# Kernel tuning notes

Measured on AMD Instinct MI355X. Metric: run time of the kernel, lower is better.

The kernel has to match this reference:

```python
import jax, jax.numpy as jnp
import numpy as np

MAX_ARMY_SEND = 64


def setup_inputs() -> dict:
    key = jax.random.key(0)
    ks = jax.random.split(key, 12)
    N, D, E = 100000, 128, 1000000
    H = 128            # hidden_dim (== embed_dim)
    AH = 128           # army_scorer hidden width (hardcoded 128 in the module)
    node_embeddings = jax.random.normal(ks[0], (N, D), dtype=jnp.float32)
    action_edges = jax.random.randint(ks[1], (E, 2), 0, N, dtype=jnp.int32)
    army_counts = jax.random.randint(ks[2], (N,), 0, 50, dtype=jnp.int32)
    s = lambda fan_in: 1.0 / np.sqrt(fan_in)
    # edge_scorer: Linear(2H -> H), ReLU, Linear(H -> 1)
    W1 = jax.random.uniform(ks[3], (2 * H, H), jnp.float32, -s(2 * H), s(2 * H))
    b1 = jnp.zeros((H,), jnp.float32)
    W2 = jax.random.uniform(ks[4], (H, 1), jnp.float32, -s(H), s(H))
    b2 = jnp.zeros((1,), jnp.float32)
    # army_scorer: Linear(2D -> 128), ReLU, Linear(128 -> max_army_send)
    A1 = jax.random.uniform(ks[5], (2 * D, AH), jnp.float32, -s(2 * D), s(2 * D))
    ab1 = jnp.zeros((AH,), jnp.float32)
    A2 = jax.random.uniform(ks[6], (AH, MAX_ARMY_SEND), jnp.float32, -s(AH), s(AH))
    ab2 = jnp.zeros((MAX_ARMY_SEND,), jnp.float32)
    return {
        "node_embeddings": node_embeddings,
        "action_edges": action_edges,
        "army_counts": army_counts,
        "W1": W1, "b1": b1, "W2": W2, "b2": b2,
        "A1": A1, "ab1": ab1, "A2": A2, "ab2": ab2,
    }


def reference(node_embeddings, action_edges, army_counts,
              W1, b1, W2, b2, A1, ab1, A2, ab2):
    src = action_edges[:, 0]
    tgt = action_edges[:, 1]
    # irregular gather: [E, 2D]
    edge_embed = jnp.concatenate([node_embeddings[src], node_embeddings[tgt]], axis=-1)
    # edge scorer MLP -> [E]
    h = jax.nn.relu(edge_embed @ W1 + b1)
    edge_logits = (h @ W2 + b2)[:, 0]
    # army scorer MLP -> [E, max_army_send]
    ha = jax.nn.relu(edge_embed @ A1 + ab1)
    army_logits = ha @ A2 + ab2
    # masking
    src_armies = army_counts[src]
    tgt_armies = army_counts[tgt]
    bad_edges = (src_armies <= 2) | (tgt_armies >= 3 * src_armies)
    edge_logits = edge_logits - bad_edges.astype(jnp.float32) * 1.0
    edge_logits = edge_logits - (src == tgt).astype(jnp.float32) * 100.0
    max_sendable = src_armies - 1                     # [E]
    army_range = jnp.arange(MAX_ARMY_SEND)[None, :]   # [1, K]
    valid_mask = army_range <= max_sendable[:, None]  # [E, K]
    army_logits = jnp.where(valid_mask, army_logits, jnp.float32(-1000000000.0))
    return edge_logits, army_logits
```

## Files before the change

kernel.cpp:

```cpp
#include <hip/hip_runtime.h>
#include <stdint.h>

typedef __bf16 bf16x8 __attribute__((ext_vector_type(8)));
typedef float floatx4 __attribute__((ext_vector_type(4)));
typedef float floatx2 __attribute__((ext_vector_type(2)));

#define LDP 136
#define LDP8 136

__device__ __forceinline__ float bf2f(unsigned short u) {
  return __uint_as_float(((unsigned)u) << 16);
}
__device__ __forceinline__ unsigned short f2bf(float f) {
  unsigned x = __float_as_uint(f);
  unsigned r = (x + 0x7fffu + ((x >> 16) & 1u)) >> 16;
  return (unsigned short)r;
}
__device__ __forceinline__ unsigned char f2fp8(float x) {
  int p = __builtin_amdgcn_cvt_pk_fp8_f32(x, 0.f, 0, false);
  return (unsigned char)(p & 0xff);
}

union LLU { uint2 u2; long long ll; };

__global__ __launch_bounds__(256) void k_convert_emb(
    const float* __restrict__ src, unsigned short* __restrict__ dst, int n4) {
  int i = blockIdx.x * 256 + threadIdx.x;
  if (i >= n4) return;
  float4 v = ((const float4*)src)[i];
  ushort4 o;
  o.x = f2bf(v.x); o.y = f2bf(v.y); o.z = f2bf(v.z); o.w = f2bf(v.w);
  ((ushort4*)dst)[i] = o;
}

__global__ __launch_bounds__(256) void k_prep_weights(
    const float* __restrict__ W1, const float* __restrict__ A1,
    const float* __restrict__ A2,
    unsigned short* __restrict__ WcatT, unsigned char* __restrict__ A2T8) {
  int idx = blockIdx.x * 256 + threadIdx.x;
  if (idx < 512 * 128) {
    int j = idx >> 7, k = idx & 127;
    float v;
    if (j < 128)      v = W1[k * 128 + j];
    else if (j < 256) v = A1[k * 128 + (j - 128)];
    else if (j < 384) v = W1[(128 + k) * 128 + (j - 256)];
    else              v = A1[(128 + k) * 128 + (j - 384)];
    WcatT[idx] = f2bf(v);
  } else if (idx < 512 * 128 + 64 * 128) {
    int i = idx - 512 * 128;
    int n = i >> 7, k = i & 127;
    A2T8[i] = f2fp8(A2[k * 64 + n]);
  }
}

__global__ __launch_bounds__(256, 3) void k_precompute(
    const unsigned short* __restrict__ emb,
    const unsigned short* __restrict__ WcatT,
    unsigned char* __restrict__ P8,
    int N) {
  __shared__ __align__(16) unsigned short a_lds[64 * LDP];
  __shared__ __align__(16) unsigned short b_lds[128 * LDP];
  const int t = threadIdx.x;
  const int m0 = (blockIdx.x >> 2) * 64;
  const int j0 = (blockIdx.x & 3) * 128;

  for (int it = 0; it < 4; ++it) {
    int i = it * 256 + t;
    int row = i >> 4, c8 = (i & 15) * 8;
    uint4 v = make_uint4(0u, 0u, 0u, 0u);
    if (m0 + row < N) v = *(const uint4*)(emb + (size_t)(m0 + row) * 128 + c8);
    *(uint4*)&a_lds[row * LDP + c8] = v;
  }
  for (int it = 0; it < 8; ++it) {
    int i = it * 256 + t;
    int jr = i >> 4, c8 = (i & 15) * 8;
    uint4 v = *(const uint4*)(WcatT + (size_t)(j0 + jr) * 128 + c8);
    *(uint4*)&b_lds[jr * LDP + c8] = v;
  }
  __syncthreads();

  const int w = t >> 6, l = t & 63;
  const int lr = l & 15, quad = l >> 4;
  floatx4 acc[8];
  for (int nt = 0; nt < 8; ++nt) acc[nt] = (floatx4){0.f, 0.f, 0.f, 0.f};
  for (int ks = 0; ks < 4; ++ks) {
    bf16x8 af = *(const bf16x8*)&a_lds[(w * 16 + lr) * LDP + ks * 32 + quad * 8];
    for (int nt = 0; nt < 8; ++nt) {
      bf16x8 bfv = *(const bf16x8*)&b_lds[(nt * 16 + lr) * LDP + ks * 32 + quad * 8];
      acc[nt] = __builtin_amdgcn_mfma_f32_16x16x32_bf16(af, bfv, acc[nt], 0, 0, 0);
    }
  }
  for (int nt = 0; nt < 8; ++nt) {
    int col = j0 + nt * 16 + lr;
    for (int r = 0; r < 4; ++r) {
      int n = m0 + w * 16 + quad * 4 + r;
      if (n < N) P8[(size_t)n * 512 + col] = f2fp8(acc[nt][r]);
    }
  }
}

__global__ __launch_bounds__(256, 6) void k_edges(
    const unsigned char* __restrict__ P8,
    const unsigned char* __restrict__ A2T8g,
    const int* __restrict__ edges,
    const int* __restrict__ army,
    const float* __restrict__ b1, const float* __restrict__ ab1,
    const float* __restrict__ W2, const float* __restrict__ b2,
    const float* __restrict__ ab2,
    float* __restrict__ out_edge,
    float* __restrict__ out_army,
    int E) {
  __shared__ __align__(16) unsigned char ha8[64 * LDP8];
  __shared__ __align__(16) unsigned char a2t8[64 * LDP8];
  __shared__ float s_b1cat[256];
  __shared__ float s_w2[128];
  __shared__ float s_ab2[64];
  __shared__ int s_army[64];
  __shared__ int s_edges[128];

  const int t = threadIdx.x;
  const int e0 = blockIdx.x * 64;

  for (int it = 0; it < 2; ++it) {
    int i = it * 256 + t;
    int n = i >> 3, c = (i & 7) * 16;
    *(uint4*)&a2t8[n * LDP8 + c] = *(const uint4*)(A2T8g + n * 128 + c);
  }
  s_b1cat[t] = (t < 128) ? b1[t] : ab1[t - 128];
  if (t < 128) {
    s_w2[t] = W2[t];
    int ei = e0 * 2 + t;
    s_edges[t] = (ei < E * 2) ? edges[ei] : 0;
  }
  if (t < 64) s_ab2[t] = ab2[t];
  __syncthreads();

  const float b2v = b2[0];
  const int lp = t & 31;
  const int eh = t >> 5;
  const int j0 = lp * 8;
  float rb[8], rw[8];
#pragma unroll
  for (int i = 0; i < 8; ++i) rb[i] = s_b1cat[j0 + i];
  if (lp < 16) {
#pragma unroll
    for (int i = 0; i < 8; ++i) rw[i] = s_w2[j0 + i];
  }
  for (int it = 0; it < 8; ++it) {
    int el = it * 8 + eh;
    if (e0 + el >= E) continue;
    int src = s_edges[el * 2];
    int tgt = s_edges[el * 2 + 1];
    uint2 us = *(const uint2*)(P8 + (size_t)src * 512 + j0);
    uint2 ut = *(const uint2*)(P8 + (size_t)tgt * 512 + 256 + j0);
    floatx2 s01 = __builtin_amdgcn_cvt_pk_f32_fp8(us.x, false);
    floatx2 s23 = __builtin_amdgcn_cvt_pk_f32_fp8(us.x, true);
    floatx2 s45 = __builtin_amdgcn_cvt_pk_f32_fp8(us.y, false);
    floatx2 s67 = __builtin_amdgcn_cvt_pk_f32_fp8(us.y, true);
    floatx2 t01 = __builtin_amdgcn_cvt_pk_f32_fp8(ut.x, false);
    floatx2 t23 = __builtin_amdgcn_cvt_pk_f32_fp8(ut.x, true);
    floatx2 t45 = __builtin_amdgcn_cvt_pk_f32_fp8(ut.y, false);
    floatx2 t67 = __builtin_amdgcn_cvt_pk_f32_fp8(ut.y, true);
    float h[8];
    h[0] = s01.x + t01.x + rb[0]; h[1] = s01.y + t01.y + rb[1];
    h[2] = s23.x + t23.x + rb[2]; h[3] = s23.y + t23.y + rb[3];
    h[4] = s45.x + t45.x + rb[4]; h[5] = s45.y + t45.y + rb[5];
    h[6] = s67.x + t67.x + rb[6]; h[7] = s67.y + t67.y + rb[7];
#pragma unroll
    for (int i = 0; i < 8; ++i) h[i] = h[i] > 0.f ? h[i] : 0.f;
    if (lp < 16) {
      float part = 0.f;
#pragma unroll
      for (int i = 0; i < 8; ++i) part += h[i] * rw[i];
      part += __shfl_down(part, 8, 16);
      part += __shfl_down(part, 4, 16);
      part += __shfl_down(part, 2, 16);
      part += __shfl_down(part, 1, 16);
      if (lp == 0) {
        int sa = army[src], ta = army[tgt];
        float logit = part + b2v;
        if (sa <= 2 || ta >= 3 * sa) logit -= 1.f;
        if (src == tgt) logit -= 100.f;
        out_edge[e0 + el] = logit;
        s_army[el] = sa;
      }
    } else {
      unsigned o0 = (unsigned)__builtin_amdgcn_cvt_pk_fp8_f32(h[0], h[1], 0, false);
      o0 = (unsigned)__builtin_amdgcn_cvt_pk_fp8_f32(h[2], h[3], (int)o0, true);
      unsigned o1 = (unsigned)__builtin_amdgcn_cvt_pk_fp8_f32(h[4], h[5], 0, false);
      o1 = (unsigned)__builtin_amdgcn_cvt_pk_fp8_f32(h[6], h[7], (int)o1, true);
      *(uint2*)&ha8[el * LDP8 + (j0 - 128)] = make_uint2(o0, o1);
    }
  }
  __syncthreads();

  const int w = t >> 6, l = t & 63;
  const int lr = l & 15, quad = l >> 4;
  floatx4 acc[4];
  for (int nt = 0; nt < 4; ++nt) acc[nt] = (floatx4){0.f, 0.f, 0.f, 0.f};
  for (int ks = 0; ks < 4; ++ks) {
    LLU av;
    av.u2 = *(const uint2*)&ha8[(w * 16 + lr) * LDP8 + ks * 32 + quad * 8];
#pragma unroll
    for (int nt = 0; nt < 4; ++nt) {
      LLU bv;
      bv.u2 = *(const uint2*)&a2t8[(nt * 16 + lr) * LDP8 + ks * 32 + quad * 8];
      acc[nt] = __builtin_amdgcn_mfma_f32_16x16x32_fp8_fp8(av.ll, bv.ll, acc[nt], 0, 0, 0);
    }
  }
#pragma unroll
  for (int nt = 0; nt < 4; ++nt) {
    int col = nt * 16 + lr;
    float bias = s_ab2[col];
#pragma unroll
    for (int r = 0; r < 4; ++r) {
      int el = w * 16 + quad * 4 + r;
      if (e0 + el >= E) continue;
      int sa = s_army[el];
      float v = acc[nt][r] + bias;
      v = (col < sa) ? v : -1e9f;
      out_army[(size_t)(e0 + el) * 64 + col] = v;
    }
  }
}

extern "C" void kernel_launch(void* const* d_in, const int* in_sizes, int n_in,
                              void* d_out, int out_size, void* d_ws, size_t ws_size,
                              hipStream_t stream) {
  const float* emb_f = (const float*)d_in[0];
  const int* edges   = (const int*)d_in[1];
  const int* army    = (const int*)d_in[2];
  const float* W1    = (const float*)d_in[3];
  const float* b1    = (const float*)d_in[4];
  const float* W2    = (const float*)d_in[5];
  const float* b2    = (const float*)d_in[6];
  const float* A1    = (const float*)d_in[7];
  const float* ab1   = (const float*)d_in[8];
  const float* A2    = (const float*)d_in[9];
  const float* ab2   = (const float*)d_in[10];

  const int N = in_sizes[0] / 128;
  const int E = in_sizes[1] / 2;

  char* ws = (char*)d_ws;
  unsigned short* emb_bf = (unsigned short*)ws;
  unsigned short* WcatT  = (unsigned short*)(ws + (size_t)N * 256);
  unsigned char*  A2T8   = (unsigned char*)(WcatT + 512 * 128);
  unsigned char*  P8     = A2T8 + 64 * 128;

  float* out_edge = (float*)d_out;
  float* out_army = out_edge + E;

  int n4 = (N * 128) / 4;
  hipLaunchKernelGGL(k_convert_emb, dim3((n4 + 255) / 256), dim3(256), 0, stream,
                     emb_f, emb_bf, n4);
  hipLaunchKernelGGL(k_prep_weights, dim3((512 * 128 + 64 * 128 + 255) / 256), dim3(256),
                     0, stream, W1, A1, A2, WcatT, A2T8);
  hipLaunchKernelGGL(k_precompute, dim3(((N + 63) / 64) * 4), dim3(256), 0, stream,
                     emb_bf, WcatT, P8, N);
  hipLaunchKernelGGL(k_edges, dim3((E + 63) / 64), dim3(256), 0, stream,
                     P8, A2T8, edges, army, b1, ab1, W2, b2, ab2,
                     out_edge, out_army, E);
}
```

Measured before the change: 459.6 us.

## Fuse embedding bf16 conversion into precompute and stage fp8 output through LDS

Removes the separate fp32-to-bf16 embedding conversion kernel and converts on load inside the precompute GEMM, saving a full write and re-read of the bf16 embedding buffer plus a launch. The fp8 results are staged in shared memory and written out as coalesced 16-byte rows instead of scattered single-byte stores. It also raises the edge kernel's occupancy hint from 6 to 8 blocks. In exchange, each of the four column blocks per row tile now re-reads and re-converts fp32 embeddings, doubling load bytes into precompute, and the higher occupancy hint may cause register spills in the edge kernel.

```diff
diff --git a/kernel.cpp b/kernel.cpp
--- a/kernel.cpp
+++ b/kernel.cpp
@@ -7,10 +7,8 @@
 
 #define LDP 136
 #define LDP8 136
-
-__device__ __forceinline__ float bf2f(unsigned short u) {
-  return __uint_as_float(((unsigned)u) << 16);
-}
+#define CST 144
+
 __device__ __forceinline__ unsigned short f2bf(float f) {
   unsigned x = __float_as_uint(f);
   unsigned r = (x + 0x7fffu + ((x >> 16) & 1u)) >> 16;
@@ -22,16 +20,6 @@
 }
 
 union LLU { uint2 u2; long long ll; };
-
-__global__ __launch_bounds__(256) void k_convert_emb(
-    const float* __restrict__ src, unsigned short* __restrict__ dst, int n4) {
-  int i = blockIdx.x * 256 + threadIdx.x;
-  if (i >= n4) return;
-  float4 v = ((const float4*)src)[i];
-  ushort4 o;
-  o.x = f2bf(v.x); o.y = f2bf(v.y); o.z = f2bf(v.z); o.w = f2bf(v.w);
-  ((ushort4*)dst)[i] = o;
-}
 
 __global__ __launch_bounds__(256) void k_prep_weights(
     const float* __restrict__ W1, const float* __restrict__ A1,
@@ -54,22 +42,27 @@
 }
 
 __global__ __launch_bounds__(256, 3) void k_precompute(
-    const unsigned short* __restrict__ emb,
+    const float* __restrict__ emb_f,
     const unsigned short* __restrict__ WcatT,
     unsigned char* __restrict__ P8,
     int N) {
-  __shared__ __align__(16) unsigned short a_lds[64 * LDP];
-  __shared__ __align__(16) unsigned short b_lds[128 * LDP];
+  __shared__ __align__(16) unsigned char smem[64 * LDP * 2 + 128 * LDP * 2];
+  unsigned short* a_lds = (unsigned short*)smem;
+  unsigned short* b_lds = (unsigned short*)(smem + 64 * LDP * 2);
+  unsigned char*  c_lds = smem;
+
   const int t = threadIdx.x;
   const int m0 = (blockIdx.x >> 2) * 64;
   const int j0 = (blockIdx.x & 3) * 128;
 
-  for (int it = 0; it < 4; ++it) {
-    int i = it * 256 + t;
-    int row = i >> 4, c8 = (i & 15) * 8;
-    uint4 v = make_uint4(0u, 0u, 0u, 0u);
-    if (m0 + row < N) v = *(const uint4*)(emb + (size_t)(m0 + row) * 128 + c8);
-    *(uint4*)&a_lds[row * LDP + c8] = v;
+  for (int it = 0; it < 8; ++it) {
+    int i = it * 256 + t;
+    int row = i >> 5, c4 = (i & 31) * 4;
+    float4 v = make_float4(0.f, 0.f, 0.f, 0.f);
+    if (m0 + row < N) v = *(const float4*)(emb_f + (size_t)(m0 + row) * 128 + c4);
+    ushort4 o;
+    o.x = f2bf(v.x); o.y = f2bf(v.y); o.z = f2bf(v.z); o.w = f2bf(v.w);
+    *(ushort4*)&a_lds[row * LDP + c4] = o;
   }
   for (int it = 0; it < 8; ++it) {
     int i = it * 256 + t;
@@ -85,21 +78,36 @@
   for (int nt = 0; nt < 8; ++nt) acc[nt] = (floatx4){0.f, 0.f, 0.f, 0.f};
   for (int ks = 0; ks < 4; ++ks) {
     bf16x8 af = *(const bf16x8*)&a_lds[(w * 16 + lr) * LDP + ks * 32 + quad * 8];
+#pragma unroll
     for (int nt = 0; nt < 8; ++nt) {
       bf16x8 bfv = *(const bf16x8*)&b_lds[(nt * 16 + lr) * LDP + ks * 32 + quad * 8];
       acc[nt] = __builtin_amdgcn_mfma_f32_16x16x32_bf16(af, bfv, acc[nt], 0, 0, 0);
     }
   }
+  __syncthreads();
+
+#pragma unroll
   for (int nt = 0; nt < 8; ++nt) {
-    int col = j0 + nt * 16 + lr;
+    int col = nt * 16 + lr;
+#pragma unroll
     for (int r = 0; r < 4; ++r) {
-      int n = m0 + w * 16 + quad * 4 + r;
-      if (n < N) P8[(size_t)n * 512 + col] = f2fp8(acc[nt][r]);
-    }
-  }
-}
-
-__global__ __launch_bounds__(256, 6) void k_edges(
+      int row = w * 16 + quad * 4 + r;
+      c_lds[row * CST + col] = f2fp8(acc[nt][r]);
+    }
+  }
+  __syncthreads();
+
+  for (int it = 0; it < 2; ++it) {
+    int i = it * 256 + t;
+    int row = i >> 3, c16 = (i & 7) * 16;
+    if (m0 + row < N) {
+      uint4 v = *(const uint4*)&c_lds[row * CST + c16];
+      *(uint4*)(P8 + (size_t)(m0 + row) * 512 + j0 + c16) = v;
+    }
+  }
+}
+
+__global__ __launch_bounds__(256, 8) void k_edges(
     const unsigned char* __restrict__ P8,
     const unsigned char* __restrict__ A2T8g,
     const int* __restrict__ edges,
@@ -243,21 +251,17 @@
   const int E = in_sizes[1] / 2;
 
   char* ws = (char*)d_ws;
-  unsigned short* emb_bf = (unsigned short*)ws;
-  unsigned short* WcatT  = (unsigned short*)(ws + (size_t)N * 256);
-  unsigned char*  A2T8   = (unsigned char*)(WcatT + 512 * 128);
-  unsigned char*  P8     = A2T8 + 64 * 128;
+  unsigned short* WcatT = (unsigned short*)ws;
+  unsigned char*  A2T8  = (unsigned char*)(WcatT + 512 * 128);
+  unsigned char*  P8    = A2T8 + 64 * 128;
 
   float* out_edge = (float*)d_out;
   float* out_army = out_edge + E;
 
-  int n4 = (N * 128) / 4;
-  hipLaunchKernelGGL(k_convert_emb, dim3((n4 + 255) / 256), dim3(256), 0, stream,
-                     emb_f, emb_bf, n4);
   hipLaunchKernelGGL(k_prep_weights, dim3((512 * 128 + 64 * 128 + 255) / 256), dim3(256),
                      0, stream, W1, A1, A2, WcatT, A2T8);
   hipLaunchKernelGGL(k_precompute, dim3(((N + 63) / 64) * 4), dim3(256), 0, stream,
-                     emb_bf, WcatT, P8, N);
+                     emb_f, WcatT, P8, N);
   hipLaunchKernelGGL(k_edges, dim3((E + 63) / 64), dim3(256), 0, stream,
                      P8, A2T8, edges, army, b1, ab1, W2, b2, ab2,
                      out_edge, out_army, E);
```

After: 476.5 us. 3.7% more time.
